# Performance work log

Measured on AMD Instinct MI355X. Metric: run time of the kernel, lower is better.

The kernel has to match this reference:

```python
import jax, jax.numpy as jnp
import numpy as np

B, N, DIM = 4, 1024, 1024
H, DH, ORDER = 16, 64, 3
MAXREL = 64
INNER = H * DH
VOCAB = 2 * MAXREL + 1
SCALE = DH ** -0.5
TOPK = int(0.25 * N)  # topk_ratio=0.25 default when top_k is None


def setup_inputs() -> dict:
    key = jax.random.key(0)
    ks = jax.random.split(key, 8)
    s = 0.02
    return {
        "x": jax.random.normal(ks[0], (B, N, DIM), jnp.float32),
        "Wqkv": jax.random.normal(ks[1], (3 * INNER, DIM), jnp.float32) * s,
        "bqkv": jnp.zeros((3 * INNER,), jnp.float32),
        "Wout": jax.random.normal(ks[2], (DIM, INNER), jnp.float32) * s,
        "bout": jnp.zeros((DIM,), jnp.float32),
        "rel_k_emb": jax.random.normal(ks[3], (VOCAB, DH), jnp.float32) * s,
        "rel_v_emb": jax.random.normal(ks[4], (VOCAB, DH), jnp.float32) * s,
        "alphas_raw": jax.random.normal(ks[5], (ORDER, H), jnp.float32) * 0.5,
    }


def reference(x, Wqkv, bqkv, Wout, bout, rel_k_emb, rel_v_emb, alphas_raw):
    b, n, _ = x.shape
    qkv = x @ Wqkv.T + bqkv  # [b, n, 3*inner]
    q, k, v = jnp.split(qkv, 3, axis=-1)
    to_heads = lambda t: t.reshape(b, n, H, DH).transpose(0, 2, 1, 3)  # b h n d
    q, k, v = to_heads(q), to_heads(k), to_heads(v)

    scores = jnp.einsum('bhid,bhjd->bhij', q, k) * SCALE

    # relative position bias on keys
    coords = jnp.arange(n)
    dist = jnp.clip(coords[:, None] - coords[None, :], -MAXREL, MAXREL) + MAXREL  # [n, n]
    rel_k = rel_k_emb[dist]  # [n, n, d]
    scores = scores + jnp.einsum('bhid,ijd->bhij', q, rel_k)

    # top-k thresholding per query row
    top_vals = jax.lax.top_k(scores, TOPK)[0]
    threshold = top_vals[..., -1:]
    scores = jnp.where(scores < threshold, -jnp.inf, scores)

    attn = jax.nn.softmax(scores, axis=-1)  # [b, h, n, n]

    rel_v = rel_v_emb[dist]  # [n, n, d]
    alphas = jax.nn.sigmoid(alphas_raw)  # [order, h]

    # monomial-basis polynomial filter: res = sum_i alpha_i * A^(i+1) V (+ relV term at i=0)
    res = jnp.zeros_like(v)
    v_curr = v
    for i in range(ORDER):
        a_v = jnp.einsum('bhij,bhjd->bhid', attn, v_curr)
        if i == 0:
            a_v = a_v + jnp.einsum('bhij,ijd->bhid', attn, rel_v)
        v_curr = a_v
        res = res + alphas[i][None, :, None, None] * v_curr

    out = res.transpose(0, 2, 1, 3).reshape(b, n, INNER)
    return out @ Wout.T + bout
```

## Files before the change

kernel.cpp:

```cpp
#include <hip/hip_runtime.h>

typedef unsigned short u16;
typedef unsigned int   u32;
typedef unsigned long long u64;
typedef __bf16 bf16x8 __attribute__((ext_vector_type(8)));
typedef float  floatx4 __attribute__((ext_vector_type(4)));

#define DEV static __device__ __forceinline__

DEV u16 f2bf(float f){ u32 x = __float_as_uint(f); return (u16)((x + 0x7fffu + ((x>>16)&1u)) >> 16); }
DEV float bf2f(u16 h){ return __uint_as_float(((u32)h)<<16); }
DEV u32 cvt_pk_bf16(float a, float b){ u32 r; asm("v_cvt_pk_bf16_f32 %0, %1, %2" : "=v"(r) : "v"(a), "v"(b)); return r; }

DEV void load_lds16(const u16* g, u16* l){
  __builtin_amdgcn_global_load_lds((const __attribute__((address_space(1))) u32*)g,
                                   (__attribute__((address_space(3))) u32*)l, 16, 0, 0);
}

DEV u32 unswz64(u32 p){
  u32 r0 = ((p>>6) ^ (p>>8)) & 1u;
  u32 b4 = ((p>>4) & 1u) ^ r0;
  u32 b5 = ((p>>5) ^ (p>>7)) & 1u;
  return (p & ~0x70u) | (b4<<4) | (b5<<5) | (r0<<6);
}
DEV bf16x8 ldfrag(const u16* base, int row, int lane){
  u32 off = ((u32)row<<6) + (((u32)lane>>4)<<4);
  off ^= (u32)(row&7)<<4;
  return *(const bf16x8*)((const char*)base + off);
}

template<int BM, int BN>
__global__ __launch_bounds__(512, 4) void gemm8(
    const u16* __restrict__ A, const u16* __restrict__ Bm, float* __restrict__ C,
    const float* __restrict__ bias, int K, int lda, int ldb, int ldc, int ncmax)
{
  constexpr int MT = (BM/2)/16;
  constexpr int NT = (BN/4)/16;
  __shared__ u16 As[BM*32];
  __shared__ u16 Bs[BN*32];

  const int tid = threadIdx.x, wid = tid>>6, lane = tid&63;
  const int m0 = blockIdx.y * BM, n0 = blockIdx.x * BN;

  const u32 g = unswz64((u32)tid*16);
  const int srow = g>>6, schunk = (g&63)>>1;
  const u16* ga0 = A  + (long long)(m0 + srow)*lda + schunk;
  const u16* gb0 = Bm + (long long)(n0 + srow)*ldb + schunk;

  u16* lA = As + (wid<<9);
  u16* lB = Bs + (wid<<9);

  const int wm = wid>>2, wn = wid&3;
  const int lr = lane&15, lq = lane>>4;

  floatx4 acc[MT][NT] = {};

  for (int k = 0; k < K; k += 32) {
    __syncthreads();
    if (BM == 128 || wid < 4) load_lds16(ga0 + k, lA);
    load_lds16(gb0 + k, lB);
    __syncthreads();
    bf16x8 af[MT];
#pragma unroll
    for (int mt=0; mt<MT; ++mt)
      af[mt] = ldfrag(As, wm*(BM/2) + mt*16 + lr, lane);
#pragma unroll
    for (int nt=0; nt<NT; ++nt) {
      bf16x8 bfr = ldfrag(Bs, wn*(BN/4) + nt*16 + lr, lane);
#pragma unroll
      for (int mt=0; mt<MT; ++mt)
        acc[mt][nt] = __builtin_amdgcn_mfma_f32_16x16x32_bf16(af[mt], bfr, acc[mt][nt], 0, 0, 0);
    }
  }

#pragma unroll
  for (int nt=0; nt<NT; ++nt) {
    const int col = n0 + wn*(BN/4) + nt*16 + lr;
    if (col < ncmax) {
      const float bv = bias ? bias[col] : 0.f;
#pragma unroll
      for (int mt=0; mt<MT; ++mt) {
#pragma unroll
        for (int r=0; r<4; ++r) {
          const int row = m0 + wm*(BM/2) + mt*16 + lq*4 + r;
          C[(long long)row*ldc + col] = acc[mt][nt][r] + bv;
        }
      }
    }
  }
}

__global__ __launch_bounds__(512, 4) void av8(
    const u16* __restrict__ P,
    const u16* __restrict__ V,
    u16* __restrict__ vout,
    float* __restrict__ resb,
    const float* __restrict__ araw, int K, int order, int accum, int wv)
{
  __shared__ u16 smem[8704];
  u16* As = smem;
  u16* Bs = smem + 2048;

  const int tid = threadIdx.x, wid = tid>>6, lane = tid&63;
  const int L = blockIdx.x;
  const int z  = (L & 7) + ((L >> 7) << 3);
  const int m0 = ((L >> 3) & 15) * 64;
  const int lr = lane&15, lq = lane>>4;

  const int sw = wid & 3;
  const u32 g = unswz64((u32)(sw*1024 + lane*16));
  const int srow = g>>6, schunk = (g&63)>>1;
  const u16* gsrc = (wid < 4)
      ? P + (long long)z*1212416 + (long long)(m0 + srow)*1184 + schunk
      : V + (long long)z*75776   + (long long)srow*1184 + schunk;
  u16* ldst = (wid < 4) ? As + (sw<<9) : Bs + (sw<<9);

  const int wm = wid>>2, wn = wid&3;
  floatx4 acc[2] = {};

  for (int k = 0; k < K; k += 32) {
    __syncthreads();
    load_lds16(gsrc + k, ldst);
    __syncthreads();
    bf16x8 bfr = ldfrag(Bs, wn*16 + lr, lane);
#pragma unroll
    for (int mt=0; mt<2; ++mt){
      bf16x8 af = ldfrag(As, wm*32 + mt*16 + lr, lane);
      acc[mt] = __builtin_amdgcn_mfma_f32_16x16x32_bf16(af, bfr, acc[mt], 0, 0, 0);
    }
  }

  const int h = z & 15;
  const float alpha = 1.f/(1.f + __expf(-araw[order*16 + h]));
  float* rb = resb + (long long)z * 65536;
  const int d = wn*16 + lr;
  __syncthreads();
#pragma unroll
  for (int mt=0; mt<2; ++mt){
#pragma unroll
    for (int r=0; r<4; ++r){
      const int row = wm*32 + mt*16 + lq*4 + r;
      const float v = acc[mt][r];
      const long long ri = (long long)(m0+row)*64 + d;
      rb[ri] = accum ? (rb[ri] + alpha*v) : (alpha*v);
      smem[d*136 + row] = f2bf(v);
    }
  }
  __syncthreads();
  if (wv){
    const int dd = tid>>3, cc = (tid&7)*8;
    u16* vp = vout + (long long)z*75776 + (long long)dd*1184 + m0 + cc;
    const u16* sp = smem + dd*136 + cc;
    uint4 uu;
    uu.x = sp[0] | ((u32)sp[1]<<16);
    uu.y = sp[2] | ((u32)sp[3]<<16);
    uu.z = sp[4] | ((u32)sp[5]<<16);
    uu.w = sp[6] | ((u32)sp[7]<<16);
    *(uint4*)(vp) = uu;
  }
}

__global__ __launch_bounds__(1024, 8) void score_topk(
    const u16* __restrict__ qF,
    const u16* __restrict__ kxF,
    u16* __restrict__ P)
{
  constexpr int SROW = 1156;
  __shared__ float sm[16*SROW];
  const int tid = threadIdx.x, wid = tid>>6, lane = tid&63;
  const int L = blockIdx.x;
  const int z  = (L & 7) + ((L >> 9) << 3);
  const int mt = (L >> 3) & 63;
  const int m0 = mt*16;
  const int lr = lane&15, lq = lane>>4;

  const u16* Aq = qF + (((long long)z*64 + mt)*6*64 + lane)*8;
  const u16* Bq = kxF + ((long long)z*80*6*64 + lane)*8;

  bf16x8 af[6];
#pragma unroll
  for (int kc=0;kc<6;++kc) af[kc] = *(const bf16x8*)(Aq + kc*512);

  const int base = wid*5;
  {
    floatx4 acc[5];
#pragma unroll
    for (int t=0;t<5;++t) acc[t] = floatx4{0.f,0.f,0.f,0.f};
#pragma unroll
    for (int t=0;t<5;++t){
      if (base + t < 73){
        const u16* bp = Bq + (long long)(base+t)*3072;
        bf16x8 b0 = *(const bf16x8*)(bp);
        bf16x8 b1 = *(const bf16x8*)(bp + 512);
        bf16x8 b2 = *(const bf16x8*)(bp + 1024);
        bf16x8 b3 = *(const bf16x8*)(bp + 1536);
        bf16x8 b4 = *(const bf16x8*)(bp + 2048);
        bf16x8 b5 = *(const bf16x8*)(bp + 2560);
        acc[t] = __builtin_amdgcn_mfma_f32_16x16x32_bf16(af[0], b0, acc[t], 0, 0, 0);
        acc[t] = __builtin_amdgcn_mfma_f32_16x16x32_bf16(af[1], b1, acc[t], 0, 0, 0);
        acc[t] = __builtin_amdgcn_mfma_f32_16x16x32_bf16(af[2], b2, acc[t], 0, 0, 0);
        acc[t] = __builtin_amdgcn_mfma_f32_16x16x32_bf16(af[3], b3, acc[t], 0, 0, 0);
        acc[t] = __builtin_amdgcn_mfma_f32_16x16x32_bf16(af[4], b4, acc[t], 0, 0, 0);
        acc[t] = __builtin_amdgcn_mfma_f32_16x16x32_bf16(af[5], b5, acc[t], 0, 0, 0);
      }
    }
#pragma unroll
    for (int t=0;t<5;++t){
      if (base + t < 73){
        const int col = (base+t)*16 + lr;
        if (col < 1153){
#pragma unroll
          for (int r=0;r<4;++r) sm[(lq*4+r)*SROW + col] = acc[t][r];
        }
      }
    }
  }
  __syncthreads();

  {
    const int row = wid;
    const int i = m0 + row;
    float* R = sm + row*SROW;

    float v[16];
#pragma unroll
    for (int x=0;x<8;++x){
      float2 f = *(const float2*)(R + x*128 + lane*2);
      v[2*x] = f.x; v[2*x+1] = f.y;
    }
#pragma unroll
    for (int x=0;x<16;++x){
      const int j = (x>>1)*128 + lane*2 + (x&1);
      int dl = i - j; dl = dl > 64 ? 64 : (dl < -64 ? -64 : dl);
      v[x] += R[1024 + dl + 64];
    }
    u32 u[16];
#pragma unroll
    for (int x=0;x<16;++x){
      u32 bb = __float_as_uint(v[x]);
      u[x] = bb ^ ((u32)((int)bb >> 31) | 0x80000000u);
    }
    u32 thr = 0;
#pragma unroll 1
    for (int bit=31; bit>=0; --bit){
      const u32 cand = thr | (1u<<bit);
      int c = 0;
#pragma unroll
      for (int x=0;x<16;++x) c += __popcll(__ballot(u[x] >= cand));
      if (c == 256){
        u32 mn = 0xFFFFFFFFu;
#pragma unroll
        for (int x=0;x<16;++x) if (u[x] >= cand && u[x] < mn) mn = u[x];
        for (int o=32;o;o>>=1){ u32 t = __shfl_xor(mn, o); mn = t < mn ? t : mn; }
        thr = mn;
        break;
      }
      if (c > 256) thr = cand;
    }
    float m = -3.0e38f;
#pragma unroll
    for (int x=0;x<16;++x) m = fmaxf(m, v[x]);
    for (int o=32;o;o>>=1) m = fmaxf(m, __shfl_xor(m, o));
    float e[16]; float Z = 0.f;
#pragma unroll
    for (int x=0;x<16;++x){
      e[x] = (u[x] >= thr) ? __expf(v[x]-m) : 0.f;
      Z += e[x];
    }
    for (int o=32;o;o>>=1) Z += __shfl_xor(Z, o);
    const float rz = 1.f / Z;

    u16* Pr = P + ((long long)z*1024 + i)*1184;
    u32* Pr32 = (u32*)Pr;
    float s0 = 0.f, s1 = 0.f;
#pragma unroll
    for (int x=0;x<8;++x){
      const float p0 = e[2*x]*rz, p1 = e[2*x+1]*rz;
      *(float2*)(R + x*128 + lane*2) = float2{p0, p1};
      Pr32[x*64 + lane] = cvt_pk_bf16(p0, p1);
      const int j0 = x*128 + lane*2;
      if (j0     >= i+64) s0 += p0;
      if (j0     <= i-64) s1 += p0;
      if (j0 + 1 >= i+64) s0 += p1;
      if (j0 + 1 <= i-64) s1 += p1;
    }
    for (int o=32;o;o>>=1){ s0 += __shfl_xor(s0,o); s1 += __shfl_xor(s1,o); }
    {
      const int t = lane + 1;
      const int j = i + 64 - t;
      const float wv = (j>=0 && j<1024) ? R[j] : 0.f;
      Pr[1024 + t] = f2bf(wv);
      if (lane < 63){
        const int t2 = lane + 65;
        const int j2 = i + 64 - t2;
        const float wv2 = (j2>=0 && j2<1024) ? R[j2] : 0.f;
        Pr[1024 + t2] = f2bf(wv2);
      }
      if (lane == 0){ Pr[1024] = f2bf(s0); Pr[1152] = f2bf(s1); }
      if (lane >= 33) Pr[1120 + lane] = 0;
    }
  }
}

__global__ __launch_bounds__(256) void planeize(const float* __restrict__ src, u16* __restrict__ dst,
                                                int total, int modeB){
  int idx = blockIdx.x*256 + threadIdx.x;
  if (idx >= total) return;
  int c = idx & 1023, r = idx >> 10;
  float v = src[idx];
  u16 hi = f2bf(v); u16 lo = f2bf(v - bf2f(hi));
  u16* d = dst + (long long)r*3072 + c;
  if (modeB){ d[0]=hi; d[1024]=hi; d[2048]=lo; }
  else      { d[0]=hi; d[1024]=lo; d[2048]=hi; }
}

__global__ __launch_bounds__(256) void build_qk(const float* __restrict__ qkv,
                                                u16* __restrict__ qF, u16* __restrict__ kxF){
  int idx = blockIdx.x*256 + threadIdx.x;
  int d = idx & 63, n = (idx>>6) & 1023, bh = idx >> 16;
  int b = bh >> 4, h = bh & 15;
  long long src = (long long)(b*1024 + n)*3072 + h*64 + d;
  float qv = qkv[src];
  float kv = qkv[src + 1024] * 0.125f;
  u16 qhi=f2bf(qv), qlo=f2bf(qv - bf2f(qhi));
  u16 khi=f2bf(kv), klo=f2bf(kv - bf2f(khi));
  const int lane = (n&15) + (((d&31)>>3)<<4);
  const int elem = d&7, kc0 = d>>5;
  u16* q = qF + ((((long long)bh*64 + (n>>4))*6*64) + lane)*8 + elem;
  q[(kc0+0)*512] = qhi; q[(kc0+2)*512] = qlo; q[(kc0+4)*512] = qhi;
  u16* kx = kxF + ((((long long)bh*80 + (n>>4))*6*64) + lane)*8 + elem;
  kx[(kc0+0)*512] = khi; kx[(kc0+2)*512] = khi; kx[(kc0+4)*512] = klo;
}

__global__ __launch_bounds__(256) void build_kxrel(const float* __restrict__ relk, u16* __restrict__ kxF){
  int idx = blockIdx.x*256 + threadIdx.x;
  int d = idx & 63, t = (idx>>6) & 255, bh = idx >> 14;
  u16 hi=0, lo=0;
  if (t < 129){ float v = relk[t*64 + d]; hi = f2bf(v); lo = f2bf(v - bf2f(hi)); }
  const int nrow = 1024 + t;
  const int lane = (t&15) + (((d&31)>>3)<<4);
  const int elem = d&7, kc0 = d>>5;
  u16* kx = kxF + ((((long long)bh*80 + (nrow>>4))*6*64) + lane)*8 + elem;
  kx[(kc0+0)*512] = hi; kx[(kc0+2)*512] = hi; kx[(kc0+4)*512] = lo;
}

__global__ __launch_bounds__(256) void build_vT(const float* __restrict__ qkv, u16* __restrict__ vA){
  __shared__ float tb[64][65];
  int bh = blockIdx.x >> 4, ntile = blockIdx.x & 15;
  int b = bh >> 4, h = bh & 15;
  int tid = threadIdx.x;
  int nl = tid >> 2, dc = (tid & 3)*16;
  const float* sp = qkv + (long long)(b*1024 + ntile*64 + nl)*3072 + 2048 + h*64 + dc;
#pragma unroll
  for (int j=0;j<16;j+=4){
    float4 f = *(const float4*)(sp + j);
    tb[dc+j+0][nl]=f.x; tb[dc+j+1][nl]=f.y; tb[dc+j+2][nl]=f.z; tb[dc+j+3][nl]=f.w;
  }
  __syncthreads();
  int d = tid >> 2, nc = (tid & 3)*16;
  u16* dp = vA + ((long long)bh*64 + d)*1184 + ntile*64 + nc;
#pragma unroll
  for (int j=0;j<16;j+=8){
    u16 a0=f2bf(tb[d][nc+j+0]), a1=f2bf(tb[d][nc+j+1]), a2=f2bf(tb[d][nc+j+2]), a3=f2bf(tb[d][nc+j+3]);
    u16 a4=f2bf(tb[d][nc+j+4]), a5=f2bf(tb[d][nc+j+5]), a6=f2bf(tb[d][nc+j+6]), a7=f2bf(tb[d][nc+j+7]);
    uint4 uu; uu.x=a0|((u32)a1<<16); uu.y=a2|((u32)a3<<16); uu.z=a4|((u32)a5<<16); uu.w=a6|((u32)a7<<16);
    *(uint4*)(dp + j) = uu;
  }
}

__global__ __launch_bounds__(256) void build_vText(const float* __restrict__ relv, u16* __restrict__ vA){
  int idx = blockIdx.x*256 + threadIdx.x;
  int t = idx % 160; int rest = idx / 160; int d = rest & 63; int bh = rest >> 6;
  u16 hv = 0;
  if (t < 129) hv = f2bf(relv[t*64 + d]);
  vA[((long long)bh*64 + d)*1184 + 1024 + t] = hv;
}

__global__ __launch_bounds__(256) void build_resS(const float* __restrict__ res, u16* __restrict__ resS){
  int idx = blockIdx.x*256 + threadIdx.x;
  int d = idx & 63, n = (idx>>6) & 1023, bh = idx >> 16;
  int b = bh >> 4, h = bh & 15;
  float v = res[idx];
  u16 hi = f2bf(v), lo = f2bf(v - bf2f(hi));
  u16* p = resS + (long long)(b*1024 + n)*3072 + h*64 + d;
  p[0]=hi; p[1024]=lo; p[2048]=hi;
}

extern "C" void kernel_launch(void* const* d_in, const int* in_sizes, int n_in,
                              void* d_out, int out_size, void* d_ws, size_t ws_size,
                              hipStream_t stream) {
  const float* x    = (const float*)d_in[0];
  const float* Wqkv = (const float*)d_in[1];
  const float* bqkv = (const float*)d_in[2];
  const float* Wout = (const float*)d_in[3];
  const float* bout = (const float*)d_in[4];
  const float* relk = (const float*)d_in[5];
  const float* relv = (const float*)d_in[6];
  const float* araw = (const float*)d_in[7];
  float* out = (float*)d_out;

  char* w = (char*)d_ws;
  size_t off = 0;
  auto take = [&](size_t bytes)->char*{ char* p = w + off; off += (bytes + 255) & ~(size_t)255; return p; };

  char* regionA = take(94371840);
  u16*   xS    = (u16*)  (regionA);
  u16*   wqS   = (u16*)  (regionA + 25165824);
  float* qkv32 = (float*)(regionA + 44040192);
  u16*   Ph    = (u16*)  (regionA);
  u16*   resS  = (u16*)  (regionA);
  u16*   woS   = (u16*)  (regionA + 25165824);
  u16*   qF    = (u16*)take(25165824);
  u16*   kxF   = (u16*)take(31457280);
  u16*   vA    = (u16*)take(9699328);
  u16*   vB    = (u16*)take(9699328);
  float* res   = (float*)take(16777216);
  (void)ws_size; (void)in_sizes; (void)n_in; (void)out_size;

  planeize<<<16384,256,0,stream>>>(x,    xS,  4194304, 0);
  planeize<<<12288,256,0,stream>>>(Wqkv, wqS, 3145728, 1);
  gemm8<128,128><<<dim3(16,32,1),512,0,stream>>>(xS, wqS, qkv32, bqkv,
      3072, 3072, 3072, 3072, 2048);
  gemm8<128,128><<<dim3(8,32,1),512,0,stream>>>(xS, wqS + (long long)2048*3072,
      qkv32 + 2048, bqkv + 2048, 1024, 3072, 3072, 3072, 1024);
  build_qk   <<<16384,256,0,stream>>>(qkv32, qF, kxF);
  build_kxrel<<<4096, 256,0,stream>>>(relk, kxF);
  build_vT   <<<1024, 256,0,stream>>>(qkv32, vA);
  build_vText<<<2560, 256,0,stream>>>(relv, vA);

  for (int half = 0; half < 2; ++half) {
    const long long zo = (long long)half * 32;
    score_topk<<<2048,1024,0,stream>>>(qF + zo*196608, kxF + zo*245760, Ph);
    av8<<<512,512,0,stream>>>(Ph, vA + zo*75776, vB + zo*75776, res + zo*65536,
        araw, 1184, 0, 0, 1);
    av8<<<512,512,0,stream>>>(Ph, vB + zo*75776, vA + zo*75776, res + zo*65536,
        araw, 1024, 1, 1, 1);
    av8<<<512,512,0,stream>>>(Ph, vA + zo*75776, vB + zo*75776, res + zo*65536,
        araw, 1024, 2, 1, 0);
  }

  build_resS<<<16384,256,0,stream>>>(res, resS);
  planeize  <<<4096, 256,0,stream>>>(Wout, woS, 1048576, 1);
  gemm8<64,128><<<dim3(8,64,1),512,0,stream>>>(resS, woS, out, bout,
      3072, 3072, 3072, 1024, 1024);
}
```

Before: 589.3 us.

## Pipeline av8 K-loop with 8-stage async LDS prefetch ring

Replaces the load-sync-compute loop in the attention-times-V kernel with an 8-deep ring of global-to-LDS async loads, waiting on vmcnt so that up to seven tiles are in flight while MFMAs consume the current tile. The goal is to hide global memory latency that the old loop exposed with a full sync every 32-wide K step. The cost is larger shared memory (64KB), which lowers occupancy from the requested 4 blocks per CU. It also assumes K is at least 256.

After: 556.5 us. 1.06x faster.

```diff
diff --git a/kernel.cpp b/kernel.cpp
--- a/kernel.cpp
+++ b/kernel.cpp
@@ -15,6 +15,14 @@
 DEV void load_lds16(const u16* g, u16* l){
   __builtin_amdgcn_global_load_lds((const __attribute__((address_space(1))) u32*)g,
                                    (__attribute__((address_space(3))) u32*)l, 16, 0, 0);
+}
+
+DEV void barrier_fenced(){
+  asm volatile("" ::: "memory");
+  __builtin_amdgcn_sched_barrier(0);
+  __builtin_amdgcn_s_barrier();
+  __builtin_amdgcn_sched_barrier(0);
+  asm volatile("" ::: "memory");
 }
 
 DEV u32 unswz64(u32 p){
@@ -97,10 +105,7 @@
     float* __restrict__ resb,
     const float* __restrict__ araw, int K, int order, int accum, int wv)
 {
-  __shared__ u16 smem[8704];
-  u16* As = smem;
-  u16* Bs = smem + 2048;
-
+  __shared__ u16 smem[32768];
   const int tid = threadIdx.x, wid = tid>>6, lane = tid&63;
   const int L = blockIdx.x;
   const int z  = (L & 7) + ((L >> 7) << 3);
@@ -113,33 +118,57 @@
   const u16* gsrc = (wid < 4)
       ? P + (long long)z*1212416 + (long long)(m0 + srow)*1184 + schunk
       : V + (long long)z*75776   + (long long)srow*1184 + schunk;
-  u16* ldst = (wid < 4) ? As + (sw<<9) : Bs + (sw<<9);
+  const int bsel = (wid < 4) ? 0 : 2048;
+  u16* ldst0 = smem + bsel + (sw<<9);
 
   const int wm = wid>>2, wn = wid&3;
+  const int wm32 = wm*32, wn16 = wn*16;
+  const int nk = K >> 5;
+
+  auto stage = [&](int p){ load_lds16(gsrc + (p<<5), ldst0 + ((p&7)<<12)); };
+
   floatx4 acc[2] = {};
 
-  for (int k = 0; k < K; k += 32) {
-    __syncthreads();
-    load_lds16(gsrc + k, ldst);
-    __syncthreads();
-    bf16x8 bfr = ldfrag(Bs, wn*16 + lr, lane);
-#pragma unroll
-    for (int mt=0; mt<2; ++mt){
-      bf16x8 af = ldfrag(As, wm*32 + mt*16 + lr, lane);
-      acc[mt] = __builtin_amdgcn_mfma_f32_16x16x32_bf16(af, bfr, acc[mt], 0, 0, 0);
-    }
-  }
+#define AV_STEP(CC, VC) do { \
+    asm volatile("s_waitcnt vmcnt(" VC ")" ::: "memory"); \
+    barrier_fenced(); \
+    const u16* Asc = smem + ((u32)(CC)<<12); \
+    const u16* Bsc = Asc + 2048; \
+    bf16x8 bfr = ldfrag(Bsc, wn16 + lr, lane); \
+    bf16x8 af0 = ldfrag(Asc, wm32 + lr, lane); \
+    bf16x8 af1 = ldfrag(Asc, wm32 + 16 + lr, lane); \
+    acc[0] = __builtin_amdgcn_mfma_f32_16x16x32_bf16(af0, bfr, acc[0], 0, 0, 0); \
+    acc[1] = __builtin_amdgcn_mfma_f32_16x16x32_bf16(af1, bfr, acc[1], 0, 0, 0); \
+    barrier_fenced(); \
+  } while(0)
+
+#pragma unroll
+  for (int p = 0; p < 8; ++p) stage(p);
+
+  for (int s = 0; s < nk - 8; ++s){
+    AV_STEP(s & 7, "7");
+    stage(s + 8);
+  }
+  AV_STEP((nk-8) & 7, "7");
+  AV_STEP((nk-7) & 7, "6");
+  AV_STEP((nk-6) & 7, "5");
+  AV_STEP((nk-5) & 7, "4");
+  AV_STEP((nk-4) & 7, "3");
+  AV_STEP((nk-3) & 7, "2");
+  AV_STEP((nk-2) & 7, "1");
+  AV_STEP((nk-1) & 7, "0");
+#undef AV_STEP
 
   const int h = z & 15;
   const float alpha = 1.f/(1.f + __expf(-araw[order*16 + h]));
   float* rb = resb + (long long)z * 65536;
-  const int d = wn*16 + lr;
+  const int d = wn16 + lr;
   __syncthreads();
 #pragma unroll
   for (int mt=0; mt<2; ++mt){
 #pragma unroll
     for (int r=0; r<4; ++r){
-      const int row = wm*32 + mt*16 + lq*4 + r;
+      const int row = wm32 + mt*16 + lq*4 + r;
       const float v = acc[mt][r];
       const long long ri = (long long)(m0+row)*64 + d;
       rb[ri] = accum ? (rb[ri] + alpha*v) : (alpha*v);
```
